# Kernel optimization log

Measured on AMD Instinct MI355X. Metric: run time of the kernel, lower is better.

## Reference

```python
import jax, jax.numpy as jnp
import numpy as np

N = 40000      # nodes (adj.size(0))
ISIZE = 64     # feature dim
K = 24         # kept kNN neighbors per node after d_cut mask
E = N * K      # learner candidate edges
E_ADJ = N * K  # GCN adjacency edges
OMEGA = 0.9
GAMMA = 2.0
D_CUT = 1.5


def setup_inputs() -> dict:
    key = jax.random.key(0)
    k = jax.random.split(key, 8)
    features = jax.random.normal(k[0], (N, ISIZE), jnp.float32)
    sc = 1.0 / np.sqrt(ISIZE)
    W1 = jax.random.normal(k[1], (ISIZE, ISIZE), jnp.float32) * sc
    b1 = jnp.zeros((ISIZE,), jnp.float32)
    W2 = jax.random.normal(k[2], (ISIZE, ISIZE), jnp.float32) * sc
    b2 = jnp.zeros((ISIZE,), jnp.float32)
    adj_row = jax.random.randint(k[3], (E_ADJ,), 0, N, dtype=jnp.int32)
    adj_col = jax.random.randint(k[4], (E_ADJ,), 0, N, dtype=jnp.int32)
    # kNN-style candidate edges: K neighbors per node, no self loops
    i_idx = jnp.repeat(jnp.arange(N, dtype=jnp.int32), K)
    j_idx = (i_idx + jax.random.randint(k[5], (E,), 1, N, dtype=jnp.int32)) % N
    # precomputed distance prior: s_d = 1/exp(gamma*(d/d_cut)^2)
    dist = jax.random.uniform(k[6], (E,), jnp.float32, 0.1, 2.0)
    s_d = jnp.exp(-GAMMA * (dist / D_CUT) ** 2)
    return {"features": features, "W1": W1, "b1": b1, "W2": W2, "b2": b2,
            "s_d": s_d, "adj_row": adj_row, "adj_col": adj_col,
            "i_idx": i_idx, "j_idx": j_idx}


def _gcn(x, W, b, row, col):
    """PyG GCNConv: symmetric norm with self loops, aggregate src=row into dst=col."""
    xw = x @ W
    deg = 1.0 + jax.ops.segment_sum(jnp.ones((row.shape[0],), jnp.float32), col,
                                    num_segments=N)
    dinv = jax.lax.rsqrt(deg)
    msg = (dinv[row] * dinv[col])[:, None] * xw[row]            # [E_ADJ, ISIZE]
    out = jax.ops.segment_sum(msg, col, num_segments=N)
    return out + (dinv * dinv)[:, None] * xw + b                # self-loop + bias


def reference(features, W1, b1, W2, b2, s_d, adj_row, adj_col, i_idx, j_idx):
    # GCN stack (nlayers=2), ReLU between layers
    h = jax.nn.relu(_gcn(features, W1, b1, adj_row, adj_col))
    h = _gcn(h, W2, b2, adj_row, adj_col)
    # F.normalize(h, p=2, dim=-1)
    h = h / jnp.maximum(jnp.linalg.norm(h, axis=-1, keepdims=True), 1e-12)
    # per-edge cosine scores, clamped at 0, blended with distance prior
    s_val = jnp.sum(h[i_idx] * h[j_idx], axis=-1)               # [E]
    s_val = jax.nn.relu(s_val)
    s_val = OMEGA * s_val + (1.0 - OMEGA) * s_d
    # SparseTensor.to_symmetric(reduce='mean'): average with reverse edge if present
    keys = i_idx * N + j_idx                                    # fits int32 (N=4e4)
    rkeys = j_idx * N + i_idx
    order = jnp.argsort(keys)
    sk = keys[order]
    pos = jnp.clip(jnp.searchsorted(sk, rkeys), 0, E - 1)
    found = sk[pos] == rkeys
    rev = order[pos]
    v_sym = jnp.where(found, 0.5 * (s_val + s_val[rev]), s_val)
    # symmetric COO: original edges + reverse copies (zeroed where reverse existed)
    rows_s = jnp.concatenate([i_idx, j_idx])                    # [2E]
    cols_s = jnp.concatenate([j_idx, i_idx])
    vals_s = jnp.concatenate([v_sym, jnp.where(found, 0.0, v_sym)])
    # normalize_adj_symm: D^{-1/2} S D^{-1/2}
    deg = jax.ops.segment_sum(vals_s, rows_s, num_segments=N)
    dinv = jnp.where(deg > 0, jax.lax.rsqrt(jnp.maximum(deg, 1e-12)), 0.0)
    vals_norm = dinv[rows_s] * vals_s * dinv[cols_s]
    return vals_norm, vals_s
```

## Files before the change

### kernel.cpp

```cpp
#include <hip/hip_runtime.h>

#define N_NODES 40000
#define ISIZE   64
#define KNN     24
#define NE      (N_NODES * KNN)
#define OMEGA   0.9f
#define CAP     64
#define NBUCK   80
#define LBUCK   10
#define BCAP    16384
#define JBCAP   16384
#define EPT     8
#define PBCH    512

__device__ __forceinline__ float bf2f(unsigned short s) {
    return __uint_as_float(((unsigned)s) << 16);
}
__device__ __forceinline__ unsigned short f2bf(float f) {
    unsigned u = __float_as_uint(f);
    u += 0x7fffu + ((u >> 16) & 1u);
    return (unsigned short)(u >> 16);
}
__device__ __forceinline__ float bflo(unsigned u) { return __uint_as_float(u << 16); }
__device__ __forceinline__ float bfhi(unsigned u) { return __uint_as_float(u & 0xffff0000u); }
__device__ __forceinline__ unsigned pack2(float lo, float hi) {
    return (unsigned)f2bf(lo) | ((unsigned)f2bf(hi) << 16);
}

__global__ void k_bin(const int* __restrict__ row, const int* __restrict__ col,
                      const int* __restrict__ j_idx,
                      int* __restrict__ bcnt, unsigned* __restrict__ bbuf,
                      unsigned* __restrict__ ovf2, int* __restrict__ ovf2_cnt,
                      int* __restrict__ jbcnt, unsigned* __restrict__ jbbuf,
                      unsigned* __restrict__ jovf, int* __restrict__ jovf_cnt) {
    __shared__ int lcnt[NBUCK];
    __shared__ int lbase[NBUCK];
    const int NB_ADJ = (NE + 256 * EPT - 1) / (256 * EPT);
    int tid = threadIdx.x;
    bool adj = (int)blockIdx.x < NB_ADJ;
    int blk = adj ? blockIdx.x : blockIdx.x - NB_ADJ;
    for (int b = tid; b < NBUCK; b += 256) lcnt[b] = 0;
    __syncthreads();
    int e0 = blk * (256 * EPT);
    int myslot[EPT]; int myb[EPT]; unsigned myp[EPT];
    for (int k = 0; k < EPT; k++) {
        int e = e0 + k * 256 + tid;
        if (e < NE) {
            int b; unsigned p;
            if (adj) { int r = row[e], c = col[e]; b = c >> 9; p = ((unsigned)r << 16) | (unsigned)c; }
            else     { int j = j_idx[e];           b = j >> 9; p = ((unsigned)(j & 511) << 20) | (unsigned)e; }
            myb[k] = b; myp[k] = p;
            myslot[k] = atomicAdd(&lcnt[b], 1);
        } else myb[k] = -1;
    }
    __syncthreads();
    int* gcnt = adj ? bcnt : jbcnt;
    for (int b = tid; b < NBUCK; b += 256)
        lbase[b] = (lcnt[b] > 0) ? atomicAdd(&gcnt[b], lcnt[b]) : 0;
    __syncthreads();
    unsigned* gbuf = adj ? bbuf : jbbuf;
    unsigned* govf = adj ? ovf2 : jovf;
    int* gocnt = adj ? ovf2_cnt : jovf_cnt;
    int capb = adj ? BCAP : JBCAP;
    for (int k = 0; k < EPT; k++) {
        if (myb[k] < 0) continue;
        int pos = lbase[myb[k]] + myslot[k];
        if (pos < capb) gbuf[myb[k] * capb + pos] = myp[k];
        else { int p = atomicAdd(gocnt, 1); govf[p] = myp[k]; }
    }
}

__global__ void k_scatter2(const unsigned* __restrict__ bbuf, const int* __restrict__ bcnt,
                           int* __restrict__ cnt, unsigned short* __restrict__ ebuf,
                           unsigned* __restrict__ ovf, int* __restrict__ ovf_cnt,
                           const unsigned* __restrict__ ovf2, const int* __restrict__ ovf2_cnt) {
    const int MAIN = 8 * LBUCK * (BCAP / PBCH);
    if ((int)blockIdx.x >= MAIN) {
        int m = ovf2_cnt[0];
        for (int t = (blockIdx.x - MAIN) * 256 + threadIdx.x; t < m; t += 8 * 256) {
            unsigned p = ovf2[t];
            int c = (int)(p & 0xffffu), r = (int)(p >> 16);
            int slot = atomicAdd(&cnt[c], 1);
            if (slot < CAP) ebuf[c * CAP + slot] = (unsigned short)r;
            else { int q = atomicAdd(ovf_cnt, 1); ovf[q] = p; }
        }
        return;
    }
    int xcd = blockIdx.x & 7;
    int t   = blockIdx.x >> 3;
    int lb  = t % LBUCK;
    int chunk = t / LBUCK;
    int b = xcd + 8 * lb;
    int n = min(bcnt[b], BCAP);
    int start = chunk * PBCH;
    if (start >= n) return;
    int end = min(start + PBCH, n);
    for (int idx = start + threadIdx.x; idx < end; idx += 256) {
        unsigned p = bbuf[b * BCAP + idx];
        int c = (int)(p & 0xffffu), r = (int)(p >> 16);
        int slot = atomicAdd(&cnt[c], 1);
        if (slot < CAP) ebuf[c * CAP + slot] = (unsigned short)r;
        else { int q = atomicAdd(ovf_cnt, 1); ovf[q] = p; }
    }
}

__global__ void k_fused1(const float* __restrict__ X, const float* __restrict__ W,
                         unsigned short* __restrict__ Y0, unsigned short* __restrict__ Y1,
                         const int* __restrict__ cnt, float* __restrict__ dinv,
                         const int* __restrict__ j_idx, unsigned char* __restrict__ revb) {
    __shared__ float sW[64 * 64];
    __shared__ float sX[32 * 64];
    const int GB = N_NODES / 32;
    const int DB = (N_NODES + 255) / 256;
    int bx = blockIdx.x;
    if (bx < GB) {
        int row0 = bx * 32;
        for (int t = threadIdx.x; t < 1024; t += 256)
            ((float4*)sW)[t] = ((const float4*)W)[t];
        for (int t = threadIdx.x; t < 512; t += 256)
            ((float4*)sX)[t] = ((const float4*)(X + row0 * 64))[t];
        __syncthreads();
        int col = threadIdx.x & 63;
        int rl  = threadIdx.x >> 6;
        for (int r = rl; r < 32; r += 4) {
            float acc = 0.0f;
#pragma unroll
            for (int kk = 0; kk < 64; kk++) acc += sX[r * 64 + kk] * sW[kk * 64 + col];
            if (col < 32) Y0[(row0 + r) * 32 + col]      = f2bf(acc);
            else          Y1[(row0 + r) * 32 + col - 32] = f2bf(acc);
        }
    } else if (bx < GB + DB) {
        int n = (bx - GB) * 256 + threadIdx.x;
        if (n < N_NODES) dinv[n] = rsqrtf(1.0f + (float)cnt[n]);
    } else {
        int t = (bx - GB - DB) * 256 + threadIdx.x;
        int e = t >> 3;
        int q = t & 7;
        int i = e / KNN;
        int j = j_idx[e];
        const int* jj = j_idx + j * KNN;
        int rt = 255;
        if (jj[q] == i) rt = q;
        if (jj[8 + q] == i) rt = min(rt, 8 + q);
        if (jj[16 + q] == i) rt = min(rt, 16 + q);
#pragma unroll
        for (int m = 1; m < 8; m <<= 1) rt = min(rt, __shfl_xor(rt, m));
        if (q == 0) revb[e] = (unsigned char)rt;
    }
}

__global__ void k_gemm2(const unsigned short* __restrict__ X, const float* __restrict__ W,
                        unsigned short* __restrict__ Y0, unsigned short* __restrict__ Y1) {
    __shared__ float sW[64 * 64];
    __shared__ float sX[32 * 64];
    int row0 = blockIdx.x * 32;
    for (int t = threadIdx.x; t < 1024; t += 256)
        ((float4*)sW)[t] = ((const float4*)W)[t];
    for (int t = threadIdx.x; t < 512; t += 256) {
        uint2 u = ((const uint2*)(X + row0 * 64))[t];
        float4 v = make_float4(bflo(u.x), bfhi(u.x), bflo(u.y), bfhi(u.y));
        ((float4*)sX)[t] = v;
    }
    __syncthreads();
    int col = threadIdx.x & 63;
    int rl  = threadIdx.x >> 6;
    for (int r = rl; r < 32; r += 4) {
        float acc = 0.0f;
#pragma unroll
        for (int kk = 0; kk < 64; kk++) acc += sX[r * 64 + kk] * sW[kk * 64 + col];
        if (col < 32) Y0[(row0 + r) * 32 + col]      = f2bf(acc);
        else          Y1[(row0 + r) * 32 + col - 32] = f2bf(acc);
    }
}

template<bool RELU, bool NORM>
__global__ void k_aggf3(const uint2* __restrict__ X0p2, const uint2* __restrict__ X1p2,
                        uint2* __restrict__ outFp2,
                        uint2* __restrict__ O0p2,
                        uint2* __restrict__ O1p2,
                        const float* __restrict__ dinv, const int* __restrict__ cnt,
                        const unsigned short* __restrict__ ebuf, const float* __restrict__ bias,
                        const unsigned* __restrict__ ovf, const int* __restrict__ ovf_cnt) {
    int w = (blockIdx.x * 256 + threadIdx.x) >> 6;
    int lane = threadIdx.x & 63;
    int half = lane >> 5, sl = lane & 31;
    int n = w * 2 + half;
    if (n >= N_NODES) return;
    int deg = cnt[n];
    int bucketed = min(deg, CAP);
    int nb0 = min(bucketed, 32);
    int nb1 = bucketed - nb0;

    int   r0v = 0, r1v = 0;
    float d0v = 0.0f, d1v = 0.0f;
    if (sl < nb0) { r0v = (int)ebuf[n * CAP + sl];      d0v = dinv[r0v]; }
    if (sl < nb1) { r1v = (int)ebuf[n * CAP + 32 + sl]; d1v = dinv[r1v]; }

    int g = sl >> 3;
    int f = sl & 7;

    float a0 = 0.f, a1 = 0.f, a2 = 0.f, a3 = 0.f;
    float a4 = 0.f, a5 = 0.f, a6 = 0.f, a7 = 0.f;
    int np0 = (nb0 + 3) >> 2;
    int np1 = (nb1 + 3) >> 2;

#pragma unroll 8
    for (int d = 0; d < np0; d++) {
        int   q = 4 * d + g;
        int   r = __shfl(r0v, q, 32);
        float c = __shfl(d0v, q, 32);
        uint2 u0 = X0p2[r * 8 + f];
        uint2 u1 = X1p2[r * 8 + f];
        a0 += c * bflo(u0.x); a1 += c * bfhi(u0.x);
        a2 += c * bflo(u0.y); a3 += c * bfhi(u0.y);
        a4 += c * bflo(u1.x); a5 += c * bfhi(u1.x);
        a6 += c * bflo(u1.y); a7 += c * bfhi(u1.y);
    }
#pragma unroll 8
    for (int d = 0; d < np1; d++) {
        int   q = 4 * d + g;
        int   r = __shfl(r1v, q, 32);
        float c = __shfl(d1v, q, 32);
        uint2 u0 = X0p2[r * 8 + f];
        uint2 u1 = X1p2[r * 8 + f];
        a0 += c * bflo(u0.x); a1 += c * bfhi(u0.x);
        a2 += c * bflo(u0.y); a3 += c * bfhi(u0.y);
        a4 += c * bflo(u1.x); a5 += c * bfhi(u1.x);
        a6 += c * bflo(u1.y); a7 += c * bfhi(u1.y);
    }

    if (deg > CAP) {
        int m = ovf_cnt[0];
        for (int k = 0; k < m; k++) {
            unsigned p = ovf[k];
            if ((int)(p & 0xffffu) == n && g == 0) {
                int r = (int)(p >> 16);
                float c = dinv[r];
                uint2 u0 = X0p2[r * 8 + f], u1 = X1p2[r * 8 + f];
                a0 += c * bflo(u0.x); a1 += c * bfhi(u0.x);
                a2 += c * bflo(u0.y); a3 += c * bfhi(u0.y);
                a4 += c * bflo(u1.x); a5 += c * bfhi(u1.x);
                a6 += c * bflo(u1.y); a7 += c * bfhi(u1.y);
            }
        }
    }

    a0 += __shfl_xor(a0, 8, 32);  a1 += __shfl_xor(a1, 8, 32);
    a2 += __shfl_xor(a2, 8, 32);  a3 += __shfl_xor(a3, 8, 32);
    a4 += __shfl_xor(a4, 8, 32);  a5 += __shfl_xor(a5, 8, 32);
    a6 += __shfl_xor(a6, 8, 32);  a7 += __shfl_xor(a7, 8, 32);
    a0 += __shfl_xor(a0, 16, 32); a1 += __shfl_xor(a1, 16, 32);
    a2 += __shfl_xor(a2, 16, 32); a3 += __shfl_xor(a3, 16, 32);
    a4 += __shfl_xor(a4, 16, 32); a5 += __shfl_xor(a5, 16, 32);
    a6 += __shfl_xor(a6, 16, 32); a7 += __shfl_xor(a7, 16, 32);

    float di = dinv[n];
    uint2 s0 = X0p2[n * 8 + f], s1 = X1p2[n * 8 + f];
    float4 bA = ((const float4*)bias)[f];
    float4 bB = ((const float4*)(bias + 32))[f];
    float dd = di * di;
    float v0 = di * a0 + dd * bflo(s0.x) + bA.x;
    float v1 = di * a1 + dd * bfhi(s0.x) + bA.y;
    float v2 = di * a2 + dd * bflo(s0.y) + bA.z;
    float v3 = di * a3 + dd * bfhi(s0.y) + bA.w;
    float v4 = di * a4 + dd * bflo(s1.x) + bB.x;
    float v5 = di * a5 + dd * bfhi(s1.x) + bB.y;
    float v6 = di * a6 + dd * bflo(s1.y) + bB.z;
    float v7 = di * a7 + dd * bfhi(s1.y) + bB.w;
    if (RELU) {
        v0 = fmaxf(v0, 0.f); v1 = fmaxf(v1, 0.f); v2 = fmaxf(v2, 0.f); v3 = fmaxf(v3, 0.f);
        v4 = fmaxf(v4, 0.f); v5 = fmaxf(v5, 0.f); v6 = fmaxf(v6, 0.f); v7 = fmaxf(v7, 0.f);
    }
    if (NORM) {
        float s = v0 * v0 + v1 * v1 + v2 * v2 + v3 * v3
                + v4 * v4 + v5 * v5 + v6 * v6 + v7 * v7;
        s += __shfl_xor(s, 1, 32); s += __shfl_xor(s, 2, 32); s += __shfl_xor(s, 4, 32);
        float inv = 1.0f / fmaxf(sqrtf(s), 1e-12f);
        v0 *= inv; v1 *= inv; v2 *= inv; v3 *= inv;
        v4 *= inv; v5 *= inv; v6 *= inv; v7 *= inv;
        if (g == 0) {
            O0p2[n * 8 + f] = make_uint2(pack2(v0, v1), pack2(v2, v3));
            O1p2[n * 8 + f] = make_uint2(pack2(v4, v5), pack2(v6, v7));
        }
    } else {
        if (g == 0) {
            outFp2[n * 16 + f]     = make_uint2(pack2(v0, v1), pack2(v2, v3));
            outFp2[n * 16 + 8 + f] = make_uint2(pack2(v4, v5), pack2(v6, v7));
        }
    }
}

__global__ void k_dot0(const uint4* __restrict__ h0q, const int* __restrict__ j_idx,
                       float* __restrict__ pdot) {
    int t = blockIdx.x * 256 + threadIdx.x;
    int e = t >> 3;
    int q = t & 7;
    int g = q >> 2, f = q & 3;
    int i = e / KNN;
    int j = j_idx[e];
    int node = g ? j : i;
    uint4 v = h0q[node * 4 + f];
    uint4 p;
    p.x = __shfl_xor(v.x, 4); p.y = __shfl_xor(v.y, 4);
    p.z = __shfl_xor(v.z, 4); p.w = __shfl_xor(v.w, 4);
    float s = bflo(v.x) * bflo(p.x) + bfhi(v.x) * bfhi(p.x)
            + bflo(v.y) * bflo(p.y) + bfhi(v.y) * bfhi(p.y)
            + bflo(v.z) * bflo(p.z) + bfhi(v.z) * bfhi(p.z)
            + bflo(v.w) * bflo(p.w) + bfhi(v.w) * bfhi(p.w);
    s += __shfl_xor(s, 1);
    s += __shfl_xor(s, 2);
    if (q == 0) pdot[e] = s;
}

__global__ void k_edgesym2(const uint4* __restrict__ h1q, const float* __restrict__ pdot,
                           const float* __restrict__ s_d, const int* __restrict__ j_idx,
                           const unsigned char* __restrict__ revb,
                           float* __restrict__ outS) {
    int t = blockIdx.x * 256 + threadIdx.x;
    int e = t >> 3;
    int q = t & 7;
    int g = q >> 2, f = q & 3;
    int i = e / KNN;
    int j = j_idx[e];
    int node = g ? j : i;
    uint4 v = h1q[node * 4 + f];
    uint4 p;
    p.x = __shfl_xor(v.x, 4); p.y = __shfl_xor(v.y, 4);
    p.z = __shfl_xor(v.z, 4); p.w = __shfl_xor(v.w, 4);
    float s = bflo(v.x) * bflo(p.x) + bfhi(v.x) * bfhi(p.x)
            + bflo(v.y) * bflo(p.y) + bfhi(v.y) * bfhi(p.y)
            + bflo(v.z) * bflo(p.z) + bfhi(v.z) * bfhi(p.z)
            + bflo(v.w) * bflo(p.w) + bfhi(v.w) * bfhi(p.w);
    s += __shfl_xor(s, 1);
    s += __shfl_xor(s, 2);
    if (q == 0) {
        s += pdot[e];
        float base = OMEGA * fmaxf(s, 0.0f);
        int rt = revb[e];
        float vv, v2;
        if (rt != 255) {
            int rev = j * KNN + rt;
            vv = base + 0.5f * (1.0f - OMEGA) * (s_d[e] + s_d[rev]);
            v2 = 0.0f;
        } else {
            vv = base + (1.0f - OMEGA) * s_d[e];
            v2 = vv;
        }
        outS[e] = vv;
        outS[NE + e] = v2;
    }
}

__global__ void k_jagg(const unsigned* __restrict__ jbbuf, const int* __restrict__ jbcnt,
                       const float* __restrict__ outS, float* __restrict__ dinv2,
                       const unsigned* __restrict__ jovf, const int* __restrict__ jovf_cnt,
                       const int* __restrict__ j_idx) {
    __shared__ float ld[512];
    int b = blockIdx.x;
    int tid = threadIdx.x;
    if (tid < 512) ld[tid] = 0.0f;
    __syncthreads();
    const float* outSv2 = outS + NE;
    int n = min(jbcnt[b], JBCAP);
    for (int idx = tid; idx < n; idx += 1024) {
        unsigned p = jbbuf[b * JBCAP + idx];
        atomicAdd(&ld[p >> 20], outSv2[p & 0xFFFFFu]);
    }
    int m = jovf_cnt[0];
    for (int t2 = tid; t2 < m; t2 += 1024) {
        int e = (int)(jovf[t2] & 0xFFFFFu);
        int j = j_idx[e];
        if ((j >> 9) == b) atomicAdd(&ld[j & 511], outSv2[e]);
    }
    __syncthreads();
    if (tid < 512) {
        int node = b * 512 + tid;
        if (node < N_NODES) {
            float d = ld[tid];
            const float* pp = outS + node * KNN;
#pragma unroll
            for (int qq = 0; qq < KNN; qq++) d += pp[qq];
            dinv2[node] = (d > 0.0f) ? rsqrtf(fmaxf(d, 1e-12f)) : 0.0f;
        }
    }
}

__global__ void k_norm(const float* __restrict__ outS, const float* __restrict__ dinv2,
                       const int* __restrict__ j_idx, float* __restrict__ out) {
    int t = blockIdx.x * 256 + threadIdx.x;
    int r, c;
    if (t < NE) { r = t / KNN; c = j_idx[t]; }
    else        { int e = t - NE; r = j_idx[e]; c = e / KNN; }
    out[t] = dinv2[r] * outS[t] * dinv2[c];
}

extern "C" void kernel_launch(void* const* d_in, const int* in_sizes, int n_in,
                              void* d_out, int out_size, void* d_ws, size_t ws_size,
                              hipStream_t stream) {
    const float* features = (const float*)d_in[0];
    const float* W1       = (const float*)d_in[1];
    const float* b1       = (const float*)d_in[2];
    const float* W2       = (const float*)d_in[3];
    const float* b2       = (const float*)d_in[4];
    const float* s_d      = (const float*)d_in[5];
    const int*   adj_row  = (const int*)d_in[6];
    const int*   adj_col  = (const int*)d_in[7];
    const int*   j_idx    = (const int*)d_in[9];
    float* out = (float*)d_out;

    const int N64 = N_NODES * 64;
    const int N32 = N_NODES * 32;
    int*   cnt     = (int*)d_ws;
    int*   ovfcnts = cnt + N_NODES;
    int*   bcnt    = ovfcnts + 16;
    int*   jbcnt   = bcnt + NBUCK;
    float* dinv    = (float*)(jbcnt + NBUCK);
    float* dinv2   = dinv + N_NODES;
    unsigned short* A0  = (unsigned short*)(dinv2 + N_NODES);
    unsigned short* A1  = A0 + N32;
    unsigned short* B16 = A1 + N32;
    unsigned short* H0  = B16 + N64;
    unsigned short* H1  = H0 + N32;
    unsigned short* ebuf = H1 + N32;
    unsigned* ovf    = (unsigned*)(ebuf + N_NODES * CAP);
    unsigned char* revb = (unsigned char*)(ovf + NE);
    unsigned* bbuf   = (unsigned*)(revb + NE);
    unsigned* jbbuf  = bbuf + NBUCK * BCAP;
    unsigned* ovf2   = jbbuf + NBUCK * JBCAP;
    unsigned* jovf   = ovf2 + NE;
    float*    pdot   = (float*)bbuf;

    size_t zero_bytes = (size_t)(N_NODES + 16 + 2 * NBUCK) * 4;
    hipMemsetAsync(cnt, 0, zero_bytes, stream);

    const int NB_ADJ = (NE + 256 * EPT - 1) / (256 * EPT);
    k_bin<<<2 * NB_ADJ, 256, 0, stream>>>(adj_row, adj_col, j_idx,
                                          bcnt, bbuf, ovf2, ovfcnts + 4,
                                          jbcnt, jbbuf, jovf, ovfcnts + 8);
    k_scatter2<<<8 * LBUCK * (BCAP / PBCH) + 8, 256, 0, stream>>>(bbuf, bcnt, cnt, ebuf,
                                                                  ovf, ovfcnts, ovf2, ovfcnts + 4);

    const int GB = N_NODES / 32, DB = (N_NODES + 255) / 256, RB = NE * 8 / 256;
    k_fused1<<<GB + DB + RB, 256, 0, stream>>>(features, W1, A0, A1, cnt, dinv, j_idx, revb);

    k_aggf3<true, false><<<(N_NODES / 2 * 64 + 255) / 256, 256, 0, stream>>>(
        (const uint2*)A0, (const uint2*)A1, (uint2*)B16, nullptr, nullptr,
        dinv, cnt, ebuf, b1, ovf, ovfcnts);

    k_gemm2<<<N_NODES / 32, 256, 0, stream>>>(B16, W2, A0, A1);
    k_aggf3<false, true><<<(N_NODES / 2 * 64 + 255) / 256, 256, 0, stream>>>(
        (const uint2*)A0, (const uint2*)A1, nullptr, (uint2*)H0, (uint2*)H1,
        dinv, cnt, ebuf, b2, ovf, ovfcnts);

    float* outS = out + 2 * NE;
    k_dot0<<<NE * 8 / 256, 256, 0, stream>>>((const uint4*)H0, j_idx, pdot);
    k_edgesym2<<<NE * 8 / 256, 256, 0, stream>>>((const uint4*)H1, pdot, s_d, j_idx, revb, outS);

    k_jagg<<<NBUCK, 1024, 0, stream>>>(jbbuf, jbcnt, outS, dinv2, jovf, ovfcnts + 8, j_idx);
    k_norm<<<2 * NE / 256, 256, 0, stream>>>(outS, dinv2, j_idx, out);
}
```

Measured before the change: 292.9 us.

## Fuse binning with first GEMM, widen aggregation loads, merge edge dot kernels

Merges the edge binning, first feature GEMM and reverse-edge lookup into one launch, since the GEMM no longer needs degree counts. Drops the precomputed dinv array and recomputes rsqrt from counts inside aggregation. Aggregation now uses 16-byte loads with 8 neighbor groups per pass. The two edge dot-product kernels are fused, so the intermediate pdot buffer is no longer written and read. Costs are more registers in aggregation and extra random reads of cnt.

```diff
diff --git a/kernel.cpp b/kernel.cpp
--- a/kernel.cpp
+++ b/kernel.cpp
@@ -27,46 +27,85 @@
     return (unsigned)f2bf(lo) | ((unsigned)f2bf(hi) << 16);
 }
 
-__global__ void k_bin(const int* __restrict__ row, const int* __restrict__ col,
-                      const int* __restrict__ j_idx,
-                      int* __restrict__ bcnt, unsigned* __restrict__ bbuf,
-                      unsigned* __restrict__ ovf2, int* __restrict__ ovf2_cnt,
-                      int* __restrict__ jbcnt, unsigned* __restrict__ jbbuf,
-                      unsigned* __restrict__ jovf, int* __restrict__ jovf_cnt) {
-    __shared__ int lcnt[NBUCK];
-    __shared__ int lbase[NBUCK];
-    const int NB_ADJ = (NE + 256 * EPT - 1) / (256 * EPT);
+__global__ void k_mega1(const float* __restrict__ X, const float* __restrict__ W,
+                        unsigned short* __restrict__ Y0, unsigned short* __restrict__ Y1,
+                        const int* __restrict__ row, const int* __restrict__ col,
+                        const int* __restrict__ j_idx,
+                        int* __restrict__ bcnt, unsigned* __restrict__ bbuf,
+                        unsigned* __restrict__ ovf2, int* __restrict__ ovf2_cnt,
+                        int* __restrict__ jbcnt, unsigned* __restrict__ jbbuf,
+                        unsigned* __restrict__ jovf, int* __restrict__ jovf_cnt,
+                        unsigned char* __restrict__ revb) {
+    __shared__ float sW[64 * 64];
+    __shared__ float sX[32 * 64];
+    const int GB  = N_NODES / 32;
+    const int NBA = (NE + 256 * EPT - 1) / (256 * EPT);
+    int bx = blockIdx.x;
     int tid = threadIdx.x;
-    bool adj = (int)blockIdx.x < NB_ADJ;
-    int blk = adj ? blockIdx.x : blockIdx.x - NB_ADJ;
-    for (int b = tid; b < NBUCK; b += 256) lcnt[b] = 0;
-    __syncthreads();
-    int e0 = blk * (256 * EPT);
-    int myslot[EPT]; int myb[EPT]; unsigned myp[EPT];
-    for (int k = 0; k < EPT; k++) {
-        int e = e0 + k * 256 + tid;
-        if (e < NE) {
-            int b; unsigned p;
-            if (adj) { int r = row[e], c = col[e]; b = c >> 9; p = ((unsigned)r << 16) | (unsigned)c; }
-            else     { int j = j_idx[e];           b = j >> 9; p = ((unsigned)(j & 511) << 20) | (unsigned)e; }
-            myb[k] = b; myp[k] = p;
-            myslot[k] = atomicAdd(&lcnt[b], 1);
-        } else myb[k] = -1;
-    }
-    __syncthreads();
-    int* gcnt = adj ? bcnt : jbcnt;
-    for (int b = tid; b < NBUCK; b += 256)
-        lbase[b] = (lcnt[b] > 0) ? atomicAdd(&gcnt[b], lcnt[b]) : 0;
-    __syncthreads();
-    unsigned* gbuf = adj ? bbuf : jbbuf;
-    unsigned* govf = adj ? ovf2 : jovf;
-    int* gocnt = adj ? ovf2_cnt : jovf_cnt;
-    int capb = adj ? BCAP : JBCAP;
-    for (int k = 0; k < EPT; k++) {
-        if (myb[k] < 0) continue;
-        int pos = lbase[myb[k]] + myslot[k];
-        if (pos < capb) gbuf[myb[k] * capb + pos] = myp[k];
-        else { int p = atomicAdd(gocnt, 1); govf[p] = myp[k]; }
+    if (bx < GB) {
+        int row0 = bx * 32;
+        for (int t = tid; t < 1024; t += 256)
+            ((float4*)sW)[t] = ((const float4*)W)[t];
+        for (int t = tid; t < 512; t += 256)
+            ((float4*)sX)[t] = ((const float4*)(X + row0 * 64))[t];
+        __syncthreads();
+        int cc = tid & 63;
+        int rl = tid >> 6;
+        for (int r = rl; r < 32; r += 4) {
+            float acc = 0.0f;
+#pragma unroll
+            for (int kk = 0; kk < 64; kk++) acc += sX[r * 64 + kk] * sW[kk * 64 + cc];
+            if (cc < 32) Y0[(row0 + r) * 32 + cc]      = f2bf(acc);
+            else         Y1[(row0 + r) * 32 + cc - 32] = f2bf(acc);
+        }
+    } else if (bx < GB + 2 * NBA) {
+        int* lcnt  = (int*)sW;
+        int* lbase = lcnt + NBUCK;
+        int blk = bx - GB;
+        bool adj = blk < NBA;
+        if (!adj) blk -= NBA;
+        for (int b = tid; b < NBUCK; b += 256) lcnt[b] = 0;
+        __syncthreads();
+        int e0 = blk * (256 * EPT);
+        int myslot[EPT]; int myb[EPT]; unsigned myp[EPT];
+        for (int k = 0; k < EPT; k++) {
+            int e = e0 + k * 256 + tid;
+            if (e < NE) {
+                int b; unsigned p;
+                if (adj) { int r = row[e], c = col[e]; b = c >> 9; p = ((unsigned)r << 16) | (unsigned)c; }
+                else     { int j = j_idx[e];           b = j >> 9; p = ((unsigned)(j & 511) << 20) | (unsigned)e; }
+                myb[k] = b; myp[k] = p;
+                myslot[k] = atomicAdd(&lcnt[b], 1);
+            } else myb[k] = -1;
+        }
+        __syncthreads();
+        int* gcnt = adj ? bcnt : jbcnt;
+        for (int b = tid; b < NBUCK; b += 256)
+            lbase[b] = (lcnt[b] > 0) ? atomicAdd(&gcnt[b], lcnt[b]) : 0;
+        __syncthreads();
+        unsigned* gbuf = adj ? bbuf : jbbuf;
+        unsigned* govf = adj ? ovf2 : jovf;
+        int* gocnt = adj ? ovf2_cnt : jovf_cnt;
+        for (int k = 0; k < EPT; k++) {
+            if (myb[k] < 0) continue;
+            int pos = lbase[myb[k]] + myslot[k];
+            if (pos < BCAP) gbuf[myb[k] * BCAP + pos] = myp[k];
+            else { int p = atomicAdd(gocnt, 1); govf[p] = myp[k]; }
+        }
+    } else {
+        int t = (bx - GB - 2 * NBA) * 256 + tid;
+        int e = t >> 3;
+        int q = t & 7;
+        int i = e / KNN;
+        int j = j_idx[e];
+        const int* jj = j_idx + j * KNN;
+        int rt = 255;
+        if (jj[q] == i) rt = q;
+        if (jj[8 + q] == i) rt = min(rt, 8 + q);
+        if (jj[16 + q] == i) rt = min(rt, 16 + q);
+#pragma unroll
+        for (int m = 1; m < 8; m <<= 1) rt = min(rt, __shfl_xor(rt, m));
+        if (q == 0) revb[e] = (unsigned char)rt;
     }
 }
 
@@ -104,51 +143,6 @@
     }
 }
 
-__global__ void k_fused1(const float* __restrict__ X, const float* __restrict__ W,
-                         unsigned short* __restrict__ Y0, unsigned short* __restrict__ Y1,
-                         const int* __restrict__ cnt, float* __restrict__ dinv,
-                         const int* __restrict__ j_idx, unsigned char* __restrict__ revb) {
-    __shared__ float sW[64 * 64];
-    __shared__ float sX[32 * 64];
-    const int GB = N_NODES / 32;
-    const int DB = (N_NODES + 255) / 256;
-    int bx = blockIdx.x;
-    if (bx < GB) {
-        int row0 = bx * 32;
-        for (int t = threadIdx.x; t < 1024; t += 256)
-            ((float4*)sW)[t] = ((const float4*)W)[t];
-        for (int t = threadIdx.x; t < 512; t += 256)
-            ((float4*)sX)[t] = ((const float4*)(X + row0 * 64))[t];
-        __syncthreads();
-        int col = threadIdx.x & 63;
-        int rl  = threadIdx.x >> 6;
-        for (int r = rl; r < 32; r += 4) {
-            float acc = 0.0f;
-#pragma unroll
-            for (int kk = 0; kk < 64; kk++) acc += sX[r * 64 + kk] * sW[kk * 64 + col];
-            if (col < 32) Y0[(row0 + r) * 32 + col]      = f2bf(acc);
-            else          Y1[(row0 + r) * 32 + col - 32] = f2bf(acc);
-        }
-    } else if (bx < GB + DB) {
-        int n = (bx - GB) * 256 + threadIdx.x;
-        if (n < N_NODES) dinv[n] = rsqrtf(1.0f + (float)cnt[n]);
-    } else {
-        int t = (bx - GB - DB) * 256 + threadIdx.x;
-        int e = t >> 3;
-        int q = t & 7;
-        int i = e / KNN;
-        int j = j_idx[e];
-        const int* jj = j_idx + j * KNN;
-        int rt = 255;
-        if (jj[q] == i) rt = q;
-        if (jj[8 + q] == i) rt = min(rt, 8 + q);
-        if (jj[16 + q] == i) rt = min(rt, 16 + q);
-#pragma unroll
-        for (int m = 1; m < 8; m <<= 1) rt = min(rt, __shfl_xor(rt, m));
-        if (q == 0) revb[e] = (unsigned char)rt;
-    }
-}
-
 __global__ void k_gemm2(const unsigned short* __restrict__ X, const float* __restrict__ W,
                         unsigned short* __restrict__ Y0, unsigned short* __restrict__ Y1) {
     __shared__ float sW[64 * 64];
@@ -158,8 +152,7 @@
         ((float4*)sW)[t] = ((const float4*)W)[t];
     for (int t = threadIdx.x; t < 512; t += 256) {
         uint2 u = ((const uint2*)(X + row0 * 64))[t];
-        float4 v = make_float4(bflo(u.x), bfhi(u.x), bflo(u.y), bfhi(u.y));
-        ((float4*)sX)[t] = v;
+        ((float4*)sX)[t] = make_float4(bflo(u.x), bfhi(u.x), bflo(u.y), bfhi(u.y));
     }
     __syncthreads();
     int col = threadIdx.x & 63;
@@ -174,11 +167,10 @@
 }
 
 template<bool RELU, bool NORM>
-__global__ void k_aggf3(const uint2* __restrict__ X0p2, const uint2* __restrict__ X1p2,
-                        uint2* __restrict__ outFp2,
-                        uint2* __restrict__ O0p2,
-                        uint2* __restrict__ O1p2,
-                        const float* __restrict__ dinv, const int* __restrict__ cnt,
+__global__ void k_aggf4(const uint4* __restrict__ X0q, const uint4* __restrict__ X1q,
+                        uint4* __restrict__ outFq,
+                        uint4* __restrict__ O0q, uint4* __restrict__ O1q,
+                        const int* __restrict__ cnt,
                         const unsigned short* __restrict__ ebuf, const float* __restrict__ bias,
                         const unsigned* __restrict__ ovf, const int* __restrict__ ovf_cnt) {
     int w = (blockIdx.x * 256 + threadIdx.x) >> 6;
@@ -193,105 +185,136 @@
 
     int   r0v = 0, r1v = 0;
     float d0v = 0.0f, d1v = 0.0f;
-    if (sl < nb0) { r0v = (int)ebuf[n * CAP + sl];      d0v = dinv[r0v]; }
-    if (sl < nb1) { r1v = (int)ebuf[n * CAP + 32 + sl]; d1v = dinv[r1v]; }
-
-    int g = sl >> 3;
-    int f = sl & 7;
-
-    float a0 = 0.f, a1 = 0.f, a2 = 0.f, a3 = 0.f;
-    float a4 = 0.f, a5 = 0.f, a6 = 0.f, a7 = 0.f;
-    int np0 = (nb0 + 3) >> 2;
-    int np1 = (nb1 + 3) >> 2;
-
-#pragma unroll 8
+    if (sl < nb0) { r0v = (int)ebuf[n * CAP + sl];      d0v = rsqrtf(1.0f + (float)cnt[r0v]); }
+    if (sl < nb1) { r1v = (int)ebuf[n * CAP + 32 + sl]; d1v = rsqrtf(1.0f + (float)cnt[r1v]); }
+
+    int g = sl >> 2;
+    int f = sl & 3;
+
+    float a[16];
+#pragma unroll
+    for (int k = 0; k < 16; k++) a[k] = 0.f;
+
+    int np0 = (nb0 + 7) >> 3;
+    int np1 = (nb1 + 7) >> 3;
+
+#pragma unroll 4
     for (int d = 0; d < np0; d++) {
-        int   q = 4 * d + g;
+        int   q = 8 * d + g;
         int   r = __shfl(r0v, q, 32);
         float c = __shfl(d0v, q, 32);
-        uint2 u0 = X0p2[r * 8 + f];
-        uint2 u1 = X1p2[r * 8 + f];
-        a0 += c * bflo(u0.x); a1 += c * bfhi(u0.x);
-        a2 += c * bflo(u0.y); a3 += c * bfhi(u0.y);
-        a4 += c * bflo(u1.x); a5 += c * bfhi(u1.x);
-        a6 += c * bflo(u1.y); a7 += c * bfhi(u1.y);
-    }
-#pragma unroll 8
+        uint4 u0 = X0q[r * 4 + f];
+        uint4 u1 = X1q[r * 4 + f];
+        a[0]  += c * bflo(u0.x); a[1]  += c * bfhi(u0.x);
+        a[2]  += c * bflo(u0.y); a[3]  += c * bfhi(u0.y);
+        a[4]  += c * bflo(u0.z); a[5]  += c * bfhi(u0.z);
+        a[6]  += c * bflo(u0.w); a[7]  += c * bfhi(u0.w);
+        a[8]  += c * bflo(u1.x); a[9]  += c * bfhi(u1.x);
+        a[10] += c * bflo(u1.y); a[11] += c * bfhi(u1.y);
+        a[12] += c * bflo(u1.z); a[13] += c * bfhi(u1.z);
+        a[14] += c * bflo(u1.w); a[15] += c * bfhi(u1.w);
+    }
+#pragma unroll 4
     for (int d = 0; d < np1; d++) {
-        int   q = 4 * d + g;
+        int   q = 8 * d + g;
         int   r = __shfl(r1v, q, 32);
         float c = __shfl(d1v, q, 32);
-        uint2 u0 = X0p2[r * 8 + f];
-        uint2 u1 = X1p2[r * 8 + f];
-        a0 += c * bflo(u0.x); a1 += c * bfhi(u0.x);
-        a2 += c * bflo(u0.y); a3 += c * bfhi(u0.y);
-        a4 += c * bflo(u1.x); a5 += c * bfhi(u1.x);
-        a6 += c * bflo(u1.y); a7 += c * bfhi(u1.y);
+        uint4 u0 = X0q[r * 4 + f];
+        uint4 u1 = X1q[r * 4 + f];
+        a[0]  += c * bflo(u0.x); a[1]  += c * bfhi(u0.x);
+        a[2]  += c * bflo(u0.y); a[3]  += c * bfhi(u0.y);
+        a[4]  += c * bflo(u0.z); a[5]  += c * bfhi(u0.z);
+        a[6]  += c * bflo(u0.w); a[7]  += c * bfhi(u0.w);
+        a[8]  += c * bflo(u1.x); a[9]  += c * bfhi(u1.x);
+        a[10] += c * bflo(u1.y); a[11] += c * bfhi(u1.y);
+        a[12] += c * bflo(u1.z); a[13] += c * bfhi(u1.z);
+        a[14] += c * bflo(u1.w); a[15] += c * bfhi(u1.w);
     }
 
     if (deg > CAP) {
         int m = ovf_cnt[0];
-        for (int k = 0; k < m; k++) {
-            unsigned p = ovf[k];
+        for (int k2 = 0; k2 < m; k2++) {
+            unsigned p = ovf[k2];
             if ((int)(p & 0xffffu) == n && g == 0) {
                 int r = (int)(p >> 16);
-                float c = dinv[r];
-                uint2 u0 = X0p2[r * 8 + f], u1 = X1p2[r * 8 + f];
-                a0 += c * bflo(u0.x); a1 += c * bfhi(u0.x);
-                a2 += c * bflo(u0.y); a3 += c * bfhi(u0.y);
-                a4 += c * bflo(u1.x); a5 += c * bfhi(u1.x);
-                a6 += c * bflo(u1.y); a7 += c * bfhi(u1.y);
+                float c = rsqrtf(1.0f + (float)cnt[r]);
+                uint4 u0 = X0q[r * 4 + f], u1 = X1q[r * 4 + f];
+                a[0]  += c * bflo(u0.x); a[1]  += c * bfhi(u0.x);
+                a[2]  += c * bflo(u0.y); a[3]  += c * bfhi(u0.y);
+                a[4]  += c * bflo(u0.z); a[5]  += c * bfhi(u0.z);
+                a[6]  += c * bflo(u0.w); a[7]  += c * bfhi(u0.w);
+                a[8]  += c * bflo(u1.x); a[9]  += c * bfhi(u1.x);
+                a[10] += c * bflo(u1.y); a[11] += c * bfhi(u1.y);
+                a[12] += c * bflo(u1.z); a[13] += c * bfhi(u1.z);
+                a[14] += c * bflo(u1.w); a[15] += c * bfhi(u1.w);
             }
         }
     }
 
-    a0 += __shfl_xor(a0, 8, 32);  a1 += __shfl_xor(a1, 8, 32);
-    a2 += __shfl_xor(a2, 8, 32);  a3 += __shfl_xor(a3, 8, 32);
-    a4 += __shfl_xor(a4, 8, 32);  a5 += __shfl_xor(a5, 8, 32);
-    a6 += __shfl_xor(a6, 8, 32);  a7 += __shfl_xor(a7, 8, 32);
-    a0 += __shfl_xor(a0, 16, 32); a1 += __shfl_xor(a1, 16, 32);
-    a2 += __shfl_xor(a2, 16, 32); a3 += __shfl_xor(a3, 16, 32);
-    a4 += __shfl_xor(a4, 16, 32); a5 += __shfl_xor(a5, 16, 32);
-    a6 += __shfl_xor(a6, 16, 32); a7 += __shfl_xor(a7, 16, 32);
-
-    float di = dinv[n];
-    uint2 s0 = X0p2[n * 8 + f], s1 = X1p2[n * 8 + f];
-    float4 bA = ((const float4*)bias)[f];
-    float4 bB = ((const float4*)(bias + 32))[f];
+#pragma unroll
+    for (int k = 0; k < 16; k++) {
+        a[k] += __shfl_xor(a[k], 4, 32);
+        a[k] += __shfl_xor(a[k], 8, 32);
+        a[k] += __shfl_xor(a[k], 16, 32);
+    }
+
+    float di = rsqrtf(1.0f + (float)deg);
     float dd = di * di;
-    float v0 = di * a0 + dd * bflo(s0.x) + bA.x;
-    float v1 = di * a1 + dd * bfhi(s0.x) + bA.y;
-    float v2 = di * a2 + dd * bflo(s0.y) + bA.z;
-    float v3 = di * a3 + dd * bfhi(s0.y) + bA.w;
-    float v4 = di * a4 + dd * bflo(s1.x) + bB.x;
-    float v5 = di * a5 + dd * bfhi(s1.x) + bB.y;
-    float v6 = di * a6 + dd * bflo(s1.y) + bB.z;
-    float v7 = di * a7 + dd * bfhi(s1.y) + bB.w;
+    uint4 s0 = X0q[n * 4 + f], s1 = X1q[n * 4 + f];
+    float4 bA0 = ((const float4*)bias)[2 * f];
+    float4 bA1 = ((const float4*)bias)[2 * f + 1];
+    float4 bB0 = ((const float4*)(bias + 32))[2 * f];
+    float4 bB1 = ((const float4*)(bias + 32))[2 * f + 1];
+    float v[16];
+    v[0]  = di * a[0]  + dd * bflo(s0.x) + bA0.x;
+    v[1]  = di * a[1]  + dd * bfhi(s0.x) + bA0.y;
+    v[2]  = di * a[2]  + dd * bflo(s0.y) + bA0.z;
+    v[3]  = di * a[3]  + dd * bfhi(s0.y) + bA0.w;
+    v[4]  = di * a[4]  + dd * bflo(s0.z) + bA1.x;
+    v[5]  = di * a[5]  + dd * bfhi(s0.z) + bA1.y;
+    v[6]  = di * a[6]  + dd * bflo(s0.w) + bA1.z;
+    v[7]  = di * a[7]  + dd * bfhi(s0.w) + bA1.w;
+    v[8]  = di * a[8]  + dd * bflo(s1.x) + bB0.x;
+    v[9]  = di * a[9]  + dd * bfhi(s1.x) + bB0.y;
+    v[10] = di * a[10] + dd * bflo(s1.y) + bB0.z;
+    v[11] = di * a[11] + dd * bfhi(s1.y) + bB0.w;
+    v[12] = di * a[12] + dd * bflo(s1.z) + bB1.x;
+    v[13] = di * a[13] + dd * bfhi(s1.z) + bB1.y;
+    v[14] = di * a[14] + dd * bflo(s1.w) + bB1.z;
+    v[15] = di * a[15] + dd * bfhi(s1.w) + bB1.w;
     if (RELU) {
-        v0 = fmaxf(v0, 0.f); v1 = fmaxf(v1, 0.f); v2 = fmaxf(v2, 0.f); v3 = fmaxf(v3, 0.f);
-        v4 = fmaxf(v4, 0.f); v5 = fmaxf(v5, 0.f); v6 = fmaxf(v6, 0.f); v7 = fmaxf(v7, 0.f);
+#pragma unroll
+        for (int k = 0; k < 16; k++) v[k] = fmaxf(v[k], 0.f);
     }
     if (NORM) {
-        float s = v0 * v0 + v1 * v1 + v2 * v2 + v3 * v3
-                + v4 * v4 + v5 * v5 + v6 * v6 + v7 * v7;
-        s += __shfl_xor(s, 1, 32); s += __shfl_xor(s, 2, 32); s += __shfl_xor(s, 4, 32);
+        float s = 0.f;
+#pragma unroll
+        for (int k = 0; k < 16; k++) s += v[k] * v[k];
+        s += __shfl_xor(s, 1, 32);
+        s += __shfl_xor(s, 2, 32);
         float inv = 1.0f / fmaxf(sqrtf(s), 1e-12f);
-        v0 *= inv; v1 *= inv; v2 *= inv; v3 *= inv;
-        v4 *= inv; v5 *= inv; v6 *= inv; v7 *= inv;
+#pragma unroll
+        for (int k = 0; k < 16; k++) v[k] *= inv;
         if (g == 0) {
-            O0p2[n * 8 + f] = make_uint2(pack2(v0, v1), pack2(v2, v3));
-            O1p2[n * 8 + f] = make_uint2(pack2(v4, v5), pack2(v6, v7));
+            O0q[n * 4 + f] = make_uint4(pack2(v[0], v[1]),  pack2(v[2], v[3]),
+                                        pack2(v[4], v[5]),  pack2(v[6], v[7]));
+            O1q[n * 4 + f] = make_uint4(pack2(v[8], v[9]),  pack2(v[10], v[11]),
+                                        pack2(v[12], v[13]), pack2(v[14], v[15]));
         }
     } else {
         if (g == 0) {
-            outFp2[n * 16 + f]     = make_uint2(pack2(v0, v1), pack2(v2, v3));
-            outFp2[n * 16 + 8 + f] = make_uint2(pack2(v4, v5), pack2(v6, v7));
-        }
-    }
-}
-
-__global__ void k_dot0(const uint4* __restrict__ h0q, const int* __restrict__ j_idx,
-                       float* __restrict__ pdot) {
+            outFq[n * 8 + f]     = make_uint4(pack2(v[0], v[1]),  pack2(v[2], v[3]),
+                                              pack2(v[4], v[5]),  pack2(v[6], v[7]));
+            outFq[n * 8 + 4 + f] = make_uint4(pack2(v[8], v[9]),  pack2(v[10], v[11]),
+                                              pack2(v[12], v[13]), pack2(v[14], v[15]));
+        }
+    }
+}
+
+__global__ void k_dotsym(const uint4* __restrict__ H0q, const uint4* __restrict__ H1q,
+                         const float* __restrict__ s_d, const int* __restrict__ j_idx,
+                         const unsigned char* __restrict__ revb,
+                         float* __restrict__ outS) {
     int t = blockIdx.x * 256 + threadIdx.x;
     int e = t >> 3;
     int q = t & 7;
@@ -299,42 +322,24 @@
     int i = e / KNN;
     int j = j_idx[e];
     int node = g ? j : i;
-    uint4 v = h0q[node * 4 + f];
-    uint4 p;
-    p.x = __shfl_xor(v.x, 4); p.y = __shfl_xor(v.y, 4);
-    p.z = __shfl_xor(v.z, 4); p.w = __shfl_xor(v.w, 4);
-    float s = bflo(v.x) * bflo(p.x) + bfhi(v.x) * bfhi(p.x)
-            + bflo(v.y) * bflo(p.y) + bfhi(v.y) * bfhi(p.y)
-            + bflo(v.z) * bflo(p.z) + bfhi(v.z) * bfhi(p.z)
-            + bflo(v.w) * bflo(p.w) + bfhi(v.w) * bfhi(p.w);
-    s += __shfl_xor(s, 1);
-    s += __shfl_xor(s, 2);
-    if (q == 0) pdot[e] = s;
-}
-
-__global__ void k_edgesym2(const uint4* __restrict__ h1q, const float* __restrict__ pdot,
-                           const float* __restrict__ s_d, const int* __restrict__ j_idx,
-                           const unsigned char* __restrict__ revb,
-                           float* __restrict__ outS) {
-    int t = blockIdx.x * 256 + threadIdx.x;
-    int e = t >> 3;
-    int q = t & 7;
-    int g = q >> 2, f = q & 3;
-    int i = e / KNN;
-    int j = j_idx[e];
-    int node = g ? j : i;
-    uint4 v = h1q[node * 4 + f];
-    uint4 p;
-    p.x = __shfl_xor(v.x, 4); p.y = __shfl_xor(v.y, 4);
-    p.z = __shfl_xor(v.z, 4); p.w = __shfl_xor(v.w, 4);
-    float s = bflo(v.x) * bflo(p.x) + bfhi(v.x) * bfhi(p.x)
-            + bflo(v.y) * bflo(p.y) + bfhi(v.y) * bfhi(p.y)
-            + bflo(v.z) * bflo(p.z) + bfhi(v.z) * bfhi(p.z)
-            + bflo(v.w) * bflo(p.w) + bfhi(v.w) * bfhi(p.w);
+    uint4 u0 = H0q[node * 4 + f];
+    uint4 u1 = H1q[node * 4 + f];
+    uint4 p0, p1;
+    p0.x = __shfl_xor(u0.x, 4); p0.y = __shfl_xor(u0.y, 4);
+    p0.z = __shfl_xor(u0.z, 4); p0.w = __shfl_xor(u0.w, 4);
+    p1.x = __shfl_xor(u1.x, 4); p1.y = __shfl_xor(u1.y, 4);
+    p1.z = __shfl_xor(u1.z, 4); p1.w = __shfl_xor(u1.w, 4);
+    float s = bflo(u0.x) * bflo(p0.x) + bfhi(u0.x) * bfhi(p0.x)
+            + bflo(u0.y) * bflo(p0.y) + bfhi(u0.y) * bfhi(p0.y)
+            + bflo(u0.z) * bflo(p0.z) + bfhi(u0.z) * bfhi(p0.z)
+            + bflo(u0.w) * bflo(p0.w) + bfhi(u0.w) * bfhi(p0.w)
+            + bflo(u1.x) * bflo(p1.x) + bfhi(u1.x) * bfhi(p1.x)
+            + bflo(u1.y) * bflo(p1.y) + bfhi(u1.y) * bfhi(p1.y)
+            + bflo(u1.z) * bflo(p1.z) + bfhi(u1.z) * bfhi(p1.z)
+            + bflo(u1.w) * bflo(p1.w) + bfhi(u1.w) * bfhi(p1.w);
     s += __shfl_xor(s, 1);
     s += __shfl_xor(s, 2);
     if (q == 0) {
-        s += pdot[e];
         float base = OMEGA * fmaxf(s, 0.0f);
         int rt = revb[e];
         float vv, v2;
@@ -414,8 +419,7 @@
     int*   ovfcnts = cnt + N_NODES;
     int*   bcnt    = ovfcnts + 16;
     int*   jbcnt   = bcnt + NBUCK;
-    float* dinv    = (float*)(jbcnt + NBUCK);
-    float* dinv2   = dinv + N_NODES;
+    float* dinv2   = (float*)(jbcnt + NBUCK);
     unsigned short* A0  = (unsigned short*)(dinv2 + N_NODES);
     unsigned short* A1  = A0 + N32;
     unsigned short* B16 = A1 + N32;
@@ -428,33 +432,32 @@
     unsigned* jbbuf  = bbuf + NBUCK * BCAP;
     unsigned* ovf2   = jbbuf + NBUCK * JBCAP;
     unsigned* jovf   = ovf2 + NE;
-    float*    pdot   = (float*)bbuf;
 
     size_t zero_bytes = (size_t)(N_NODES + 16 + 2 * NBUCK) * 4;
     hipMemsetAsync(cnt, 0, zero_bytes, stream);
 
-    const int NB_ADJ = (NE + 256 * EPT - 1) / (256 * EPT);
-    k_bin<<<2 * NB_ADJ, 256, 0, stream>>>(adj_row, adj_col, j_idx,
-                                          bcnt, bbuf, ovf2, ovfcnts + 4,
-                                          jbcnt, jbbuf, jovf, ovfcnts + 8);
-    k_scatter2<<<8 * LBUCK * (BCAP / PBCH) + 8, 256, 0, stream>>>(bbuf, bcnt, cnt, ebuf,
-                                                                  ovf, ovfcnts, ovf2, ovfcnts + 4);
-
-    const int GB = N_NODES / 32, DB = (N_NODES + 255) / 256, RB = NE * 8 / 256;
-    k_fused1<<<GB + DB + RB, 256, 0, stream>>>(features, W1, A0, A1, cnt, dinv, j_idx, revb);
-
-    k_aggf3<true, false><<<(N_NODES / 2 * 64 + 255) / 256, 256, 0, stream>>>(
-        (const uint2*)A0, (const uint2*)A1, (uint2*)B16, nullptr, nullptr,
-        dinv, cnt, ebuf, b1, ovf, ovfcnts);
+    const int GB = N_NODES / 32;
+    const int NBA = (NE + 256 * EPT - 1) / (256 * EPT);
+    const int RB = NE * 8 / 256;
+    k_mega1<<<GB + 2 * NBA + RB, 256, 0, stream>>>(
+        features, W1, A0, A1, adj_row, adj_col, j_idx,
+        bcnt, bbuf, ovf2, ovfcnts + 4, jbcnt, jbbuf, jovf, ovfcnts + 8, revb);
+
+    k_scatter2<<<8 * LBUCK * (BCAP / PBCH) + 8, 256, 0, stream>>>(
+        bbuf, bcnt, cnt, ebuf, ovf, ovfcnts, ovf2, ovfcnts + 4);
+
+    k_aggf4<true, false><<<(N_NODES / 2 * 64 + 255) / 256, 256, 0, stream>>>(
+        (const uint4*)A0, (const uint4*)A1, (uint4*)B16, nullptr, nullptr,
+        cnt, ebuf, b1, ovf, ovfcnts);
 
     k_gemm2<<<N_NODES / 32, 256, 0, stream>>>(B16, W2, A0, A1);
-    k_aggf3<false, true><<<(N_NODES / 2 * 64 + 255) / 256, 256, 0, stream>>>(
-        (const uint2*)A0, (const uint2*)A1, nullptr, (uint2*)H0, (uint2*)H1,
-        dinv, cnt, ebuf, b2, ovf, ovfcnts);
+    k_aggf4<false, true><<<(N_NODES / 2 * 64 + 255) / 256, 256, 0, stream>>>(
+        (const uint4*)A0, (const uint4*)A1, nullptr, (uint4*)H0, (uint4*)H1,
+        cnt, ebuf, b2, ovf, ovfcnts);
 
     float* outS = out + 2 * NE;
-    k_dot0<<<NE * 8 / 256, 256, 0, stream>>>((const uint4*)H0, j_idx, pdot);
-    k_edgesym2<<<NE * 8 / 256, 256, 0, stream>>>((const uint4*)H1, pdot, s_d, j_idx, revb, outS);
+    k_dotsym<<<NE * 8 / 256, 256, 0, stream>>>(
+        (const uint4*)H0, (const uint4*)H1, s_d, j_idx, revb, outS);
 
     k_jagg<<<NBUCK, 1024, 0, stream>>>(jbbuf, jbcnt, outS, dinv2, jovf, ovfcnts + 8, j_idx);
     k_norm<<<2 * NE / 256, 256, 0, stream>>>(outS, dinv2, j_idx, out);
```

New measurement: 271.6 us. 1.08x faster.
